# Kernel tuning notes

Hardware: AMD Instinct MI355X
Metric: run time of the kernel (lower is better)

Reference implementation:

```python
import jax, jax.numpy as jnp
import numpy as np
import math

M, INPUT_DIM, CLASSES, LATENT = 4096, 64, 10, 2

# ---- Bessel-approximation phi functions (Abramowitz & Stegun polynomial series) ----

def phi_f(s):
    t = s / 7.5
    t2 = t * t
    poly = 1.0 + 3.5156229 * t2 + 3.0899424 * t2**2 + 1.2067492 * t2**3 \
         + 0.2659732 * t2**4 + 0.0360768 * t2**5 + 0.0045813 * t2**6
    return jnp.exp(-s / 2.0) * poly


def phi_g(s):
    t = s / 7.5
    u = 1.0 / t  # s >= 7.5 when called via phi, so t >= 1
    poly = 0.39894228 + 0.01328592 * u + 0.00225319 * u**2 - 0.00157565 * u**3 \
         + 0.0091628 * u**4 - 0.02057706 * u**5 + 0.02635537 * u**6 \
         - 0.01647633 * u**7 + 0.00392377 * u**8
    return jnp.sqrt(2.0 / s) * poly


def phi(x):
    a = jnp.float32(7.5)
    return phi_f(jnp.minimum(x, a)) - phi_f(a) + phi_g(jnp.maximum(x, a))


def phi_d(s, D):
    if D <= 2:
        return phi(s)
    return 1.0 / jnp.sqrt(1.0 + 4.0 * s / (2 * D - 3))


def cramer_wold_distance(X, mu, variance, p, gamma):
    m, K = X.shape
    variance_matrix = variance[None, :] + variance[:, None]          # [C, C]
    # A term: pairwise latent-sample distances [m, m]
    A1 = jnp.sum((X[None, :, :] - X[:, None, :]) ** 2, axis=-1)      # [m, m]
    A = jnp.sum(phi_d(A1 / (4.0 * gamma), K)) / (m * m * math.sqrt(2.0 * math.pi * 2.0 * gamma))
    # B term: sample-to-mean distances [m, C]
    B1 = jnp.sum((mu[None, :, :] - X[:, None, :]) ** 2, axis=-1)     # [m, C]
    B2 = phi_d(B1 / (2.0 * (variance + 2.0 * gamma)), K)
    B = jnp.sum(2.0 * p / (m * jnp.sqrt(2.0 * math.pi * (variance + 2.0 * gamma))) * B2)
    # C term: mean-to-mean distances [C, C]
    C1 = jnp.sum((mu[None, :, :] - mu[:, None, :]) ** 2, axis=-1)
    C2 = phi_d(C1 / (2.0 * variance_matrix + 4.0 * gamma), K)
    C3 = jnp.outer(p, p) / jnp.sqrt(2.0 * math.pi * (variance_matrix + 2.0 * gamma))
    C = jnp.sum(C3 * C2)
    return A - B + C


def setup_inputs() -> dict:
    key = jax.random.key(0)
    ks = jax.random.split(key, 12)
    tau = jax.random.normal(ks[0], (M, INPUT_DIM), dtype=jnp.float32)
    # first half of batch is labeled (one-hot), second half unlabeled (zeros)
    lab_idx = jax.random.randint(ks[1], (M // 2,), 0, CLASSES)
    labels = jnp.concatenate([jax.nn.one_hot(lab_idx, CLASSES, dtype=jnp.float32),
                              jnp.zeros((M - M // 2, CLASSES), jnp.float32)], axis=0)
    batch_data = jnp.concatenate([tau, labels], axis=1)

    def xavier(k, fan_in, fan_out):
        lim = math.sqrt(6.0 / (fan_in + fan_out))
        return jax.random.uniform(k, (fan_in, fan_out), jnp.float32, -lim, lim)

    inp = {
        'batch_data': batch_data,
        'We1': xavier(ks[2], INPUT_DIM, 32), 'be1': jnp.zeros((32,), jnp.float32),
        'We2': xavier(ks[3], 32, 16),        'be2': jnp.zeros((16,), jnp.float32),
        'We3': xavier(ks[4], 16, LATENT),    'be3': jnp.zeros((LATENT,), jnp.float32),
        'Wd1': xavier(ks[5], LATENT, 16),    'bd1': jnp.zeros((16,), jnp.float32),
        'Wd2': xavier(ks[6], 16, 32),        'bd2': jnp.zeros((32,), jnp.float32),
        'Wd3': xavier(ks[7], 32, INPUT_DIM), 'bd3': jnp.zeros((INPUT_DIM,), jnp.float32),
        # GMM: init=2.0, gauss_num <= z_dim branch not taken (10 > 2) -> N(0, init)
        'means': 2.0 * jax.random.normal(ks[8], (CLASSES, LATENT), jnp.float32),
        'variances': jnp.ones((CLASSES,), jnp.float32),
        'probs': jnp.full((CLASSES,), 1.0 / CLASSES, jnp.float32),
    }
    return inp


def segma_forward(batch_data, We1, be1, We2, be2, We3, be3,
                  Wd1, bd1, Wd2, bd2, Wd3, bd3, means, variances, probs):
    tau = batch_data[:, :INPUT_DIM]
    labels = batch_data[:, INPUT_DIM:]
    # encoder
    x = jnp.tanh(tau @ We1 + be1)
    x = jnp.tanh(x @ We2 + be2)
    z = x @ We3 + be3                                               # [m, K]
    # decoder
    h = jnp.tanh(z @ Wd1 + bd1)
    h = jnp.tanh(h @ Wd2 + bd2)
    tau_decoded = h @ Wd3 + bd3
    rec_loss = jnp.mean((tau - tau_decoded) ** 2)
    # labeled mask: rows whose one-hot labels sum to exactly 1
    labeled_mask = (jnp.sum(labels, axis=-1) == 1.0)
    # class logits: Gaussian log-likelihood under each mixture component
    D = means.shape[-1]
    sq = jnp.sum((z[:, None, :] - means[None, :, :]) ** 2, axis=-1)  # [m, C]
    class_logits = jnp.log(probs) - 0.5 * D * jnp.log(2.0 * math.pi * variances) - sq / (2.0 * variances)
    # cross-entropy with (soft/one-hot) float targets, masked to labeled rows
    ce = -jnp.sum(labels * jax.nn.log_softmax(class_logits, axis=-1), axis=-1)
    den = jnp.sum(labels)
    den = jnp.where(den == 0, 1.0, den)
    class_loss = jnp.sum(ce * labeled_mask.astype(jnp.float32)) / den
    # Cramer-Wold cost (train_labeled=True -> use all z)
    m = z.shape[0]
    gamma = jnp.float32((4.0 / (3.0 * m)) ** 0.2)
    cw_cost = cramer_wold_distance(z, means, variances, probs, gamma)
    log_cw_cost = 8.0 + jnp.log(cw_cost)
    total_loss = rec_loss + 1.0 * log_cw_cost + 2.0 * class_loss
    return total_loss


def reference(batch_data, We1, be1, We2, be2, We3, be3,
              Wd1, bd1, Wd2, bd2, Wd3, bd3, means, variances, probs):
    return segma_forward(batch_data, We1, be1, We2, be2, We3, be3,
                         Wd1, bd1, Wd2, bd2, Wd3, bd3, means, variances, probs)
```

## Files before the change

### kernel.cpp

```cpp
#include <hip/hip_runtime.h>
#include <math.h>

#define M_ROWS 4096
#define IN_DIM 64
#define NCLS 10
#define ROW_STRIDE 74
#define TWO_PI_F 6.283185307179586f
#define NTILE 64
#define NPAIR 2080
#define NBLK_MLP 256

__device__ __forceinline__ float phi_f_eval(float s) {
    float t = s * (1.0f / 7.5f);
    float t2 = t * t;
    float p = 0.0045813f;
    p = fmaf(p, t2, 0.0360768f);
    p = fmaf(p, t2, 0.2659732f);
    p = fmaf(p, t2, 1.2067492f);
    p = fmaf(p, t2, 3.0899424f);
    p = fmaf(p, t2, 3.5156229f);
    p = fmaf(p, t2, 1.0f);
    return __expf(-0.5f * s) * p;
}

__device__ __forceinline__ float phi_g_eval(float s) {
    float r = __builtin_amdgcn_rcpf(s);
    float u = 7.5f * r;
    float p = 0.00392377f;
    p = fmaf(p, u, -0.01647633f);
    p = fmaf(p, u, 0.02635537f);
    p = fmaf(p, u, -0.02057706f);
    p = fmaf(p, u, 0.0091628f);
    p = fmaf(p, u, -0.00157565f);
    p = fmaf(p, u, 0.00225319f);
    p = fmaf(p, u, 0.01328592f);
    p = fmaf(p, u, 0.39894228f);
    return __builtin_amdgcn_sqrtf(2.0f * r) * p;
}

#define PHI_F_75 0.21445709f

__device__ __forceinline__ float phi_eval(float s) {
    float f = phi_f_eval(fminf(s, 7.5f));
    float g = phi_g_eval(fmaxf(s, 7.5f));
    return f - PHI_F_75 + g;
}

__device__ __forceinline__ float fast_tanh(float x) {
    float e = __expf(2.0f * x);
    float r = __builtin_amdgcn_rcpf(e + 1.0f);
    return fmaf(-2.0f, r, 1.0f);
}

__device__ __forceinline__ float waveReduce(float v) {
    v += __shfl_down(v, 32, 64);
    v += __shfl_down(v, 16, 64);
    v += __shfl_down(v, 8, 64);
    v += __shfl_down(v, 4, 64);
    v += __shfl_down(v, 2, 64);
    v += __shfl_down(v, 1, 64);
    return v;
}

__device__ __forceinline__ double waveReduceD(double v) {
    v += __shfl_down(v, 32, 64);
    v += __shfl_down(v, 16, 64);
    v += __shfl_down(v, 8, 64);
    v += __shfl_down(v, 4, 64);
    v += __shfl_down(v, 2, 64);
    v += __shfl_down(v, 1, 64);
    return v;
}

__device__ __forceinline__ float sel4(float v0, float v1, float v2, float v3, int r) {
    float a = (r & 1) ? v1 : v0;
    float b = (r & 1) ? v3 : v2;
    return (r & 2) ? b : a;
}

#define P_W1   0
#define P_W2   2304
#define P_WD2  2944
#define P_WD3  3520
#define P_W3   5696
#define P_WD1  5728
#define P_B1   5760
#define P_B2   5792
#define P_B3   5808
#define P_BD1  5810
#define P_BD2  5826
#define P_BD3  5858
#define P_MU   5922
#define P_VAR  5942
#define P_PRB  5952
#define SMT    5962

__global__ __launch_bounds__(64, 1) void k_mlp(
    const float* __restrict__ batch,
    const float* __restrict__ We1, const float* __restrict__ be1,
    const float* __restrict__ We2, const float* __restrict__ be2,
    const float* __restrict__ We3, const float* __restrict__ be3,
    const float* __restrict__ Wd1, const float* __restrict__ bd1,
    const float* __restrict__ Wd2, const float* __restrict__ bd2,
    const float* __restrict__ Wd3, const float* __restrict__ bd3,
    const float* __restrict__ means, const float* __restrict__ vars,
    const float* __restrict__ probs,
    float2* __restrict__ zbuf,
    float* __restrict__ recp, float* __restrict__ Bp,
    float* __restrict__ clsp, float* __restrict__ labp,
    float gamma)
{
    __shared__ __align__(16) float sm[SMT];
    const int tid = threadIdx.x;

    for (int idx = tid; idx < 2048; idx += 64) { int i = idx >> 5, j = idx & 31; sm[P_W1  + i * 36 + j] = We1[idx]; }
    for (int idx = tid; idx < 512;  idx += 64) { int i = idx >> 4, j = idx & 15; sm[P_W2  + i * 20 + j] = We2[idx]; }
    for (int idx = tid; idx < 512;  idx += 64) { int i = idx >> 5, j = idx & 31; sm[P_WD2 + i * 36 + j] = Wd2[idx]; }
    for (int idx = tid; idx < 2048; idx += 64) { int i = idx >> 6, j = idx & 63; sm[P_WD3 + i * 68 + j] = Wd3[idx]; }
    if (tid < 32) sm[P_W3 + tid] = We3[tid];
    else          sm[P_WD1 + tid - 32] = Wd1[tid - 32];
    if (tid < 32) sm[P_B1 + tid] = be1[tid];
    if (tid < 16) sm[P_B2 + tid] = be2[tid];
    if (tid < 2)  sm[P_B3 + tid] = be3[tid];
    if (tid < 16) sm[P_BD1 + tid] = bd1[tid];
    if (tid < 32) sm[P_BD2 + tid] = bd2[tid];
    sm[P_BD3 + tid] = bd3[tid];
    if (tid < 20) sm[P_MU + tid] = means[tid];
    if (tid < 10) sm[P_VAR + tid] = vars[tid];
    if (tid < 10) sm[P_PRB + tid] = probs[tid];
    __syncthreads();

    const int rw = tid & 15;
    const int r  = tid >> 4;
    const int row = blockIdx.x * 16 + rw;
    const float* rp = batch + (size_t)row * ROW_STRIDE;

    float taus[16];
#pragma unroll
    for (int k = 0; k < 16; k++) taus[k] = rp[r + 4 * k];

    float a1[32];
#pragma unroll
    for (int j = 0; j < 32; j++) a1[j] = 0.0f;
#pragma unroll
    for (int k = 0; k < 16; k++) {
        const int i = r + 4 * k;
        const float4* wr = (const float4*)&sm[P_W1 + i * 36];
        const float ti = taus[k];
#pragma unroll
        for (int jj = 0; jj < 8; jj++) {
            float4 w = wr[jj];
            a1[4 * jj + 0] = fmaf(ti, w.x, a1[4 * jj + 0]);
            a1[4 * jj + 1] = fmaf(ti, w.y, a1[4 * jj + 1]);
            a1[4 * jj + 2] = fmaf(ti, w.z, a1[4 * jj + 2]);
            a1[4 * jj + 3] = fmaf(ti, w.w, a1[4 * jj + 3]);
        }
    }
#pragma unroll
    for (int j = 0; j < 32; j++) {
        a1[j] += __shfl_xor(a1[j], 16, 64);
        a1[j] += __shfl_xor(a1[j], 32, 64);
    }
    float x1own[8];
#pragma unroll
    for (int k = 0; k < 8; k++)
        x1own[k] = fast_tanh(sel4(a1[4 * k], a1[4 * k + 1], a1[4 * k + 2], a1[4 * k + 3], r)
                             + sm[P_B1 + r + 4 * k]);

    float a2[16];
#pragma unroll
    for (int j = 0; j < 16; j++) a2[j] = 0.0f;
#pragma unroll
    for (int k = 0; k < 8; k++) {
        const int i = r + 4 * k;
        const float4* wr = (const float4*)&sm[P_W2 + i * 20];
        const float x = x1own[k];
#pragma unroll
        for (int jj = 0; jj < 4; jj++) {
            float4 w = wr[jj];
            a2[4 * jj + 0] = fmaf(x, w.x, a2[4 * jj + 0]);
            a2[4 * jj + 1] = fmaf(x, w.y, a2[4 * jj + 1]);
            a2[4 * jj + 2] = fmaf(x, w.z, a2[4 * jj + 2]);
            a2[4 * jj + 3] = fmaf(x, w.w, a2[4 * jj + 3]);
        }
    }
#pragma unroll
    for (int j = 0; j < 16; j++) {
        a2[j] += __shfl_xor(a2[j], 16, 64);
        a2[j] += __shfl_xor(a2[j], 32, 64);
    }
    float x2own[4];
#pragma unroll
    for (int k = 0; k < 4; k++)
        x2own[k] = fast_tanh(sel4(a2[4 * k], a2[4 * k + 1], a2[4 * k + 2], a2[4 * k + 3], r)
                             + sm[P_B2 + r + 4 * k]);

    float z0 = 0.0f, z1 = 0.0f;
#pragma unroll
    for (int k = 0; k < 4; k++) {
        const int i = r + 4 * k;
        z0 = fmaf(x2own[k], sm[P_W3 + 2 * i], z0);
        z1 = fmaf(x2own[k], sm[P_W3 + 2 * i + 1], z1);
    }
    z0 += __shfl_xor(z0, 16, 64); z0 += __shfl_xor(z0, 32, 64);
    z1 += __shfl_xor(z1, 16, 64); z1 += __shfl_xor(z1, 32, 64);
    z0 += sm[P_B3 + 0];
    z1 += sm[P_B3 + 1];
    if (r == 0) zbuf[row] = make_float2(z0, z1);

    float h1own[4];
#pragma unroll
    for (int k = 0; k < 4; k++) {
        const int j = r + 4 * k;
        float acc = sm[P_BD1 + j];
        acc = fmaf(z0, sm[P_WD1 + j], acc);
        acc = fmaf(z1, sm[P_WD1 + 16 + j], acc);
        h1own[k] = fast_tanh(acc);
    }

    float a3[32];
#pragma unroll
    for (int j = 0; j < 32; j++) a3[j] = 0.0f;
#pragma unroll
    for (int k = 0; k < 4; k++) {
        const int i = r + 4 * k;
        const float4* wr = (const float4*)&sm[P_WD2 + i * 36];
        const float x = h1own[k];
#pragma unroll
        for (int jj = 0; jj < 8; jj++) {
            float4 w = wr[jj];
            a3[4 * jj + 0] = fmaf(x, w.x, a3[4 * jj + 0]);
            a3[4 * jj + 1] = fmaf(x, w.y, a3[4 * jj + 1]);
            a3[4 * jj + 2] = fmaf(x, w.z, a3[4 * jj + 2]);
            a3[4 * jj + 3] = fmaf(x, w.w, a3[4 * jj + 3]);
        }
    }
#pragma unroll
    for (int j = 0; j < 32; j++) {
        a3[j] += __shfl_xor(a3[j], 16, 64);
        a3[j] += __shfl_xor(a3[j], 32, 64);
    }
    float h2own[8];
#pragma unroll
    for (int k = 0; k < 8; k++)
        h2own[k] = fast_tanh(sel4(a3[4 * k], a3[4 * k + 1], a3[4 * k + 2], a3[4 * k + 3], r)
                             + sm[P_BD2 + r + 4 * k]);

    float a4[64];
#pragma unroll
    for (int j = 0; j < 64; j++) a4[j] = 0.0f;
#pragma unroll
    for (int k = 0; k < 8; k++) {
        const int i = r + 4 * k;
        const float4* wr = (const float4*)&sm[P_WD3 + i * 68];
        const float x = h2own[k];
#pragma unroll
        for (int jj = 0; jj < 16; jj++) {
            float4 w = wr[jj];
            a4[4 * jj + 0] = fmaf(x, w.x, a4[4 * jj + 0]);
            a4[4 * jj + 1] = fmaf(x, w.y, a4[4 * jj + 1]);
            a4[4 * jj + 2] = fmaf(x, w.z, a4[4 * jj + 2]);
            a4[4 * jj + 3] = fmaf(x, w.w, a4[4 * jj + 3]);
        }
    }
#pragma unroll
    for (int j = 0; j < 64; j++) {
        a4[j] += __shfl_xor(a4[j], 16, 64);
        a4[j] += __shfl_xor(a4[j], 32, 64);
    }
    float rec = 0.0f;
#pragma unroll
    for (int k = 0; k < 16; k++) {
        float dec = sel4(a4[4 * k], a4[4 * k + 1], a4[4 * k + 2], a4[4 * k + 3], r)
                    + sm[P_BD3 + r + 4 * k];
        float e = dec - taus[k];
        rec = fmaf(e, e, rec);
    }

    const float two_g = 2.0f * gamma;
    const float inv_m = 1.0f / (float)M_ROWS;
    float lg[NCLS];
    float mx = -3.0e38f;
    float Bacc = 0.0f;
#pragma unroll
    for (int c = 0; c < NCLS; c++) {
        float d0 = z0 - sm[P_MU + 2 * c];
        float d1 = z1 - sm[P_MU + 2 * c + 1];
        float sqc = fmaf(d0, d0, d1 * d1);
        float vc = sm[P_VAR + c];
        float lgc = __logf(sm[P_PRB + c]) - __logf(TWO_PI_F * vc)
                    - sqc * 0.5f * __builtin_amdgcn_rcpf(vc);
        lg[c] = lgc;
        mx = fmaxf(mx, lgc);

        float den = vc + two_g;
        float sB = sqc * 0.5f * __builtin_amdgcn_rcpf(den);
        float coef = 2.0f * inv_m * sm[P_PRB + c] * __builtin_amdgcn_rsqf(TWO_PI_F * den);
        Bacc = fmaf(coef, phi_eval(sB), Bacc);
    }
    float esum = 0.0f;
#pragma unroll
    for (int c = 0; c < NCLS; c++) esum += __expf(lg[c] - mx);
    float lse = __logf(esum) + mx;

    float suml = 0.0f, ce = 0.0f;
#pragma unroll
    for (int c = 0; c < NCLS; c++) {
        float lb = rp[IN_DIM + c];
        suml += lb;
        ce = fmaf(lb, lse - lg[c], ce);
    }
    float cls = (suml == 1.0f) ? ce : 0.0f;
    if (r != 0) { Bacc = 0.0f; cls = 0.0f; suml = 0.0f; }

    float r0 = waveReduce(rec);
    float r1 = waveReduce(Bacc);
    float r2 = waveReduce(cls);
    float r3 = waveReduce(suml);
    if (tid == 0) {
        recp[blockIdx.x] = r0;
        Bp[blockIdx.x]   = r1;
        clsp[blockIdx.x] = r2;
        labp[blockIdx.x] = r3;
    }
}

__global__ __launch_bounds__(64, 4) void k_pair(
    const float2* __restrict__ z, float* __restrict__ Apart, float inv4g)
{
    const int p = blockIdx.x;
    int tj = (int)((__builtin_amdgcn_sqrtf(8.0f * (float)p + 1.0f) - 1.0f) * 0.5f);
    while ((tj + 1) * (tj + 2) / 2 <= p) tj++;
    while (tj * (tj + 1) / 2 > p) tj--;
    const int ti = p - tj * (tj + 1) / 2;

    const int lane = threadIdx.x;
    __shared__ float2 zjs[64];
    float2 zi = z[ti * 64 + lane];
    zjs[lane] = z[tj * 64 + lane];
    __syncthreads();

    float acc0 = 0.0f, acc1 = 0.0f;
#pragma unroll 8
    for (int jj = 0; jj < 64; jj += 2) {
        float2 a = zjs[jj], b = zjs[jj + 1];
        float dx0 = zi.x - a.x, dy0 = zi.y - a.y;
        float dx1 = zi.x - b.x, dy1 = zi.y - b.y;
        acc0 += phi_eval(fmaf(dx0, dx0, dy0 * dy0) * inv4g);
        acc1 += phi_eval(fmaf(dx1, dx1, dy1 * dy1) * inv4g);
    }
    float tot = waveReduce(acc0 + acc1);
    if (lane == 0) Apart[p] = (ti == tj) ? tot : 2.0f * tot;
}

__global__ __launch_bounds__(256) void k_fin(
    const float* __restrict__ means, const float* __restrict__ vars,
    const float* __restrict__ probs,
    const float* __restrict__ Apart,
    const float* __restrict__ recp, const float* __restrict__ Bp,
    const float* __restrict__ clsp, const float* __restrict__ labp,
    float* __restrict__ out, float gamma)
{
    __shared__ double wsum[8];
    const int t = threadIdx.x;
    const int w = t >> 6;
    const int l = t & 63;

    const double m = (double)M_ROWS;
    const double gam = (double)gamma;
    const double invA = 1.0 / (m * m * sqrt(2.0 * M_PI * 2.0 * gam));

    double av = 0.0;
#pragma unroll
    for (int k = 0; k < 9; k++) {
        int idx = t + 256 * k;
        if (idx < NPAIR) av += (double)Apart[idx];
    }

    double cv = 0.0;
    if (t < 100) {
        int ci = t / 10, cj = t - 10 * (t / 10);
        float vm = vars[ci] + vars[cj];
        float d0 = means[2 * ci] - means[2 * cj];
        float d1 = means[2 * ci + 1] - means[2 * cj + 1];
        float c1 = fmaf(d0, d0, d1 * d1);
        float s = c1 / (2.0f * vm + 4.0f * gamma);
        float c2 = phi_eval(s);
        float c3 = probs[ci] * probs[cj] * __builtin_amdgcn_rsqf(TWO_PI_F * (vm + 2.0f * gamma));
        cv = (double)(c3 * c2);
    }

    double acw = waveReduceD(av * invA + cv);

    const float* arr = (w == 0) ? recp : (w == 1) ? Bp : (w == 2) ? clsp : labp;
    double pv = 0.0;
#pragma unroll
    for (int k = 0; k < 4; k++) pv += (double)arr[l + 64 * k];
    double pw = waveReduceD(pv);

    if (l == 0) { wsum[w] = acw; wsum[4 + w] = pw; }
    __syncthreads();

    if (t == 0) {
        double AC = wsum[0] + wsum[1] + wsum[2] + wsum[3];
        double rec = wsum[4], B = wsum[5], cls = wsum[6], lab = wsum[7];
        double den = (lab == 0.0) ? 1.0 : lab;
        double cw = AC - B;
        double total = rec / (m * 64.0) + 8.0 + log(cw) + 2.0 * (cls / den);
        out[0] = (float)total;
    }
}

extern "C" void kernel_launch(void* const* d_in, const int* in_sizes, int n_in,
                              void* d_out, int out_size, void* d_ws, size_t ws_size,
                              hipStream_t stream) {
    (void)in_sizes; (void)n_in; (void)out_size; (void)ws_size;
    const float* batch = (const float*)d_in[0];
    const float* We1 = (const float*)d_in[1];
    const float* be1 = (const float*)d_in[2];
    const float* We2 = (const float*)d_in[3];
    const float* be2 = (const float*)d_in[4];
    const float* We3 = (const float*)d_in[5];
    const float* be3 = (const float*)d_in[6];
    const float* Wd1 = (const float*)d_in[7];
    const float* bd1 = (const float*)d_in[8];
    const float* Wd2 = (const float*)d_in[9];
    const float* bd2 = (const float*)d_in[10];
    const float* Wd3 = (const float*)d_in[11];
    const float* bd3 = (const float*)d_in[12];
    const float* means = (const float*)d_in[13];
    const float* vars = (const float*)d_in[14];
    const float* probs = (const float*)d_in[15];

    float* ws = (float*)d_ws;
    float2* zbuf = (float2*)ws;
    float* Apart = ws + 8192;
    float* recp  = ws + 12288;
    float* Bp    = ws + 12544;
    float* clsp  = ws + 12800;
    float* labp  = ws + 13056;

    const float gamma = (float)pow(4.0 / (3.0 * (double)M_ROWS), 0.2);
    const float inv4g = 1.0f / (4.0f * gamma);

    k_mlp<<<NBLK_MLP, 64, 0, stream>>>(batch, We1, be1, We2, be2, We3, be3,
                                       Wd1, bd1, Wd2, bd2, Wd3, bd3,
                                       means, vars, probs,
                                       zbuf, recp, Bp, clsp, labp, gamma);
    k_pair<<<NPAIR, 64, 0, stream>>>(zbuf, Apart, inv4g);
    k_fin<<<1, 256, 0, stream>>>(means, vars, probs, Apart, recp, Bp, clsp, labp,
                                 (float*)d_out, gamma);
}
```

Before: 116.9 us.

## Split MLP rows across 8 lane groups and fold final reduction into pair kernel

The MLP kernel now handles 8 rows per block across 512 blocks instead of 16 rows across 256, so each lane group reduces over 8 partial sums with an extra shuffle stage. The per-row class and B-term math now runs only on the owner lanes. The separate finalize kernel is removed: the last pair block, detected with an atomic counter reset by the MLP kernel, does the global reduction, saving one kernel launch. This adds atomics and fences, more shuffle traffic per block, and a single-wave tail reduction over all partials.

New measurement: 155.3 us. 1.33x slower.

```diff
diff --git a/kernel.cpp b/kernel.cpp
--- a/kernel.cpp
+++ b/kernel.cpp
@@ -6,9 +6,8 @@
 #define NCLS 10
 #define ROW_STRIDE 74
 #define TWO_PI_F 6.283185307179586f
-#define NTILE 64
 #define NPAIR 2080
-#define NBLK_MLP 256
+#define NBLK_MLP 512
 
 __device__ __forceinline__ float phi_f_eval(float s) {
     float t = s * (1.0f / 7.5f);
@@ -76,6 +75,12 @@
     float a = (r & 1) ? v1 : v0;
     float b = (r & 1) ? v3 : v2;
     return (r & 2) ? b : a;
+}
+__device__ __forceinline__ float sel8(float v0, float v1, float v2, float v3,
+                                      float v4, float v5, float v6, float v7, int r) {
+    float a = sel4(v0, v1, v2, v3, r);
+    float b = sel4(v4, v5, v6, v7, r);
+    return (r & 4) ? b : a;
 }
 
 #define P_W1   0
@@ -108,10 +113,13 @@
     float2* __restrict__ zbuf,
     float* __restrict__ recp, float* __restrict__ Bp,
     float* __restrict__ clsp, float* __restrict__ labp,
+    int* __restrict__ cnt,
     float gamma)
 {
     __shared__ __align__(16) float sm[SMT];
     const int tid = threadIdx.x;
+
+    if (blockIdx.x == 0 && tid == 0) *cnt = 0;
 
     for (int idx = tid; idx < 2048; idx += 64) { int i = idx >> 5, j = idx & 31; sm[P_W1  + i * 36 + j] = We1[idx]; }
     for (int idx = tid; idx < 512;  idx += 64) { int i = idx >> 4, j = idx & 15; sm[P_W2  + i * 20 + j] = We2[idx]; }
@@ -130,21 +138,21 @@
     if (tid < 10) sm[P_PRB + tid] = probs[tid];
     __syncthreads();
 
-    const int rw = tid & 15;
-    const int r  = tid >> 4;
-    const int row = blockIdx.x * 16 + rw;
+    const int rw = tid & 7;
+    const int r  = tid >> 3;
+    const int row = blockIdx.x * 8 + rw;
     const float* rp = batch + (size_t)row * ROW_STRIDE;
 
-    float taus[16];
-#pragma unroll
-    for (int k = 0; k < 16; k++) taus[k] = rp[r + 4 * k];
+    float taus[8];
+#pragma unroll
+    for (int k = 0; k < 8; k++) taus[k] = rp[r + 8 * k];
 
     float a1[32];
 #pragma unroll
     for (int j = 0; j < 32; j++) a1[j] = 0.0f;
 #pragma unroll
-    for (int k = 0; k < 16; k++) {
-        const int i = r + 4 * k;
+    for (int k = 0; k < 8; k++) {
+        const int i = r + 8 * k;
         const float4* wr = (const float4*)&sm[P_W1 + i * 36];
         const float ti = taus[k];
 #pragma unroll
@@ -158,21 +166,23 @@
     }
 #pragma unroll
     for (int j = 0; j < 32; j++) {
+        a1[j] += __shfl_xor(a1[j], 8, 64);
         a1[j] += __shfl_xor(a1[j], 16, 64);
         a1[j] += __shfl_xor(a1[j], 32, 64);
     }
-    float x1own[8];
-#pragma unroll
-    for (int k = 0; k < 8; k++)
-        x1own[k] = fast_tanh(sel4(a1[4 * k], a1[4 * k + 1], a1[4 * k + 2], a1[4 * k + 3], r)
-                             + sm[P_B1 + r + 4 * k]);
+    float x1own[4];
+#pragma unroll
+    for (int k = 0; k < 4; k++)
+        x1own[k] = fast_tanh(sel8(a1[8 * k], a1[8 * k + 1], a1[8 * k + 2], a1[8 * k + 3],
+                                  a1[8 * k + 4], a1[8 * k + 5], a1[8 * k + 6], a1[8 * k + 7], r)
+                             + sm[P_B1 + r + 8 * k]);
 
     float a2[16];
 #pragma unroll
     for (int j = 0; j < 16; j++) a2[j] = 0.0f;
 #pragma unroll
-    for (int k = 0; k < 8; k++) {
-        const int i = r + 4 * k;
+    for (int k = 0; k < 4; k++) {
+        const int i = r + 8 * k;
         const float4* wr = (const float4*)&sm[P_W2 + i * 20];
         const float x = x1own[k];
 #pragma unroll
@@ -186,32 +196,34 @@
     }
 #pragma unroll
     for (int j = 0; j < 16; j++) {
+        a2[j] += __shfl_xor(a2[j], 8, 64);
         a2[j] += __shfl_xor(a2[j], 16, 64);
         a2[j] += __shfl_xor(a2[j], 32, 64);
     }
-    float x2own[4];
-#pragma unroll
-    for (int k = 0; k < 4; k++)
-        x2own[k] = fast_tanh(sel4(a2[4 * k], a2[4 * k + 1], a2[4 * k + 2], a2[4 * k + 3], r)
-                             + sm[P_B2 + r + 4 * k]);
+    float x2own[2];
+#pragma unroll
+    for (int k = 0; k < 2; k++)
+        x2own[k] = fast_tanh(sel8(a2[8 * k], a2[8 * k + 1], a2[8 * k + 2], a2[8 * k + 3],
+                                  a2[8 * k + 4], a2[8 * k + 5], a2[8 * k + 6], a2[8 * k + 7], r)
+                             + sm[P_B2 + r + 8 * k]);
 
     float z0 = 0.0f, z1 = 0.0f;
 #pragma unroll
-    for (int k = 0; k < 4; k++) {
-        const int i = r + 4 * k;
+    for (int k = 0; k < 2; k++) {
+        const int i = r + 8 * k;
         z0 = fmaf(x2own[k], sm[P_W3 + 2 * i], z0);
         z1 = fmaf(x2own[k], sm[P_W3 + 2 * i + 1], z1);
     }
-    z0 += __shfl_xor(z0, 16, 64); z0 += __shfl_xor(z0, 32, 64);
-    z1 += __shfl_xor(z1, 16, 64); z1 += __shfl_xor(z1, 32, 64);
+    z0 += __shfl_xor(z0, 8, 64); z0 += __shfl_xor(z0, 16, 64); z0 += __shfl_xor(z0, 32, 64);
+    z1 += __shfl_xor(z1, 8, 64); z1 += __shfl_xor(z1, 16, 64); z1 += __shfl_xor(z1, 32, 64);
     z0 += sm[P_B3 + 0];
     z1 += sm[P_B3 + 1];
     if (r == 0) zbuf[row] = make_float2(z0, z1);
 
-    float h1own[4];
-#pragma unroll
-    for (int k = 0; k < 4; k++) {
-        const int j = r + 4 * k;
+    float h1own[2];
+#pragma unroll
+    for (int k = 0; k < 2; k++) {
+        const int j = r + 8 * k;
         float acc = sm[P_BD1 + j];
         acc = fmaf(z0, sm[P_WD1 + j], acc);
         acc = fmaf(z1, sm[P_WD1 + 16 + j], acc);
@@ -222,8 +234,8 @@
 #pragma unroll
     for (int j = 0; j < 32; j++) a3[j] = 0.0f;
 #pragma unroll
-    for (int k = 0; k < 4; k++) {
-        const int i = r + 4 * k;
+    for (int k = 0; k < 2; k++) {
+        const int i = r + 8 * k;
         const float4* wr = (const float4*)&sm[P_WD2 + i * 36];
         const float x = h1own[k];
 #pragma unroll
@@ -237,21 +249,23 @@
     }
 #pragma unroll
     for (int j = 0; j < 32; j++) {
+        a3[j] += __shfl_xor(a3[j], 8, 64);
         a3[j] += __shfl_xor(a3[j], 16, 64);
         a3[j] += __shfl_xor(a3[j], 32, 64);
     }
-    float h2own[8];
-#pragma unroll
-    for (int k = 0; k < 8; k++)
-        h2own[k] = fast_tanh(sel4(a3[4 * k], a3[4 * k + 1], a3[4 * k + 2], a3[4 * k + 3], r)
-                             + sm[P_BD2 + r + 4 * k]);
+    float h2own[4];
+#pragma unroll
+    for (int k = 0; k < 4; k++)
+        h2own[k] = fast_tanh(sel8(a3[8 * k], a3[8 * k + 1], a3[8 * k + 2], a3[8 * k + 3],
+                                  a3[8 * k + 4], a3[8 * k + 5], a3[8 * k + 6], a3[8 * k + 7], r)
+                             + sm[P_BD2 + r + 8 * k]);
 
     float a4[64];
 #pragma unroll
     for (int j = 0; j < 64; j++) a4[j] = 0.0f;
 #pragma unroll
-    for (int k = 0; k < 8; k++) {
-        const int i = r + 4 * k;
+    for (int k = 0; k < 4; k++) {
+        const int i = r + 8 * k;
         const float4* wr = (const float4*)&sm[P_WD3 + i * 68];
         const float x = h2own[k];
 #pragma unroll
@@ -265,53 +279,56 @@
     }
 #pragma unroll
     for (int j = 0; j < 64; j++) {
+        a4[j] += __shfl_xor(a4[j], 8, 64);
         a4[j] += __shfl_xor(a4[j], 16, 64);
         a4[j] += __shfl_xor(a4[j], 32, 64);
     }
     float rec = 0.0f;
 #pragma unroll
-    for (int k = 0; k < 16; k++) {
-        float dec = sel4(a4[4 * k], a4[4 * k + 1], a4[4 * k + 2], a4[4 * k + 3], r)
-                    + sm[P_BD3 + r + 4 * k];
+    for (int k = 0; k < 8; k++) {
+        float dec = sel8(a4[8 * k], a4[8 * k + 1], a4[8 * k + 2], a4[8 * k + 3],
+                         a4[8 * k + 4], a4[8 * k + 5], a4[8 * k + 6], a4[8 * k + 7], r)
+                    + sm[P_BD3 + r + 8 * k];
         float e = dec - taus[k];
         rec = fmaf(e, e, rec);
     }
 
-    const float two_g = 2.0f * gamma;
-    const float inv_m = 1.0f / (float)M_ROWS;
-    float lg[NCLS];
-    float mx = -3.0e38f;
-    float Bacc = 0.0f;
-#pragma unroll
-    for (int c = 0; c < NCLS; c++) {
-        float d0 = z0 - sm[P_MU + 2 * c];
-        float d1 = z1 - sm[P_MU + 2 * c + 1];
-        float sqc = fmaf(d0, d0, d1 * d1);
-        float vc = sm[P_VAR + c];
-        float lgc = __logf(sm[P_PRB + c]) - __logf(TWO_PI_F * vc)
-                    - sqc * 0.5f * __builtin_amdgcn_rcpf(vc);
-        lg[c] = lgc;
-        mx = fmaxf(mx, lgc);
-
-        float den = vc + two_g;
-        float sB = sqc * 0.5f * __builtin_amdgcn_rcpf(den);
-        float coef = 2.0f * inv_m * sm[P_PRB + c] * __builtin_amdgcn_rsqf(TWO_PI_F * den);
-        Bacc = fmaf(coef, phi_eval(sB), Bacc);
-    }
-    float esum = 0.0f;
-#pragma unroll
-    for (int c = 0; c < NCLS; c++) esum += __expf(lg[c] - mx);
-    float lse = __logf(esum) + mx;
-
-    float suml = 0.0f, ce = 0.0f;
-#pragma unroll
-    for (int c = 0; c < NCLS; c++) {
-        float lb = rp[IN_DIM + c];
-        suml += lb;
-        ce = fmaf(lb, lse - lg[c], ce);
-    }
-    float cls = (suml == 1.0f) ? ce : 0.0f;
-    if (r != 0) { Bacc = 0.0f; cls = 0.0f; suml = 0.0f; }
+    float Bacc = 0.0f, cls = 0.0f, suml = 0.0f;
+    if (r == 0) {
+        const float two_g = 2.0f * gamma;
+        const float inv_m = 1.0f / (float)M_ROWS;
+        float lg[NCLS];
+        float mx = -3.0e38f;
+#pragma unroll
+        for (int c = 0; c < NCLS; c++) {
+            float d0 = z0 - sm[P_MU + 2 * c];
+            float d1 = z1 - sm[P_MU + 2 * c + 1];
+            float sqc = fmaf(d0, d0, d1 * d1);
+            float vc = sm[P_VAR + c];
+            float lgc = __logf(sm[P_PRB + c]) - __logf(TWO_PI_F * vc)
+                        - sqc * 0.5f * __builtin_amdgcn_rcpf(vc);
+            lg[c] = lgc;
+            mx = fmaxf(mx, lgc);
+
+            float den = vc + two_g;
+            float sB = sqc * 0.5f * __builtin_amdgcn_rcpf(den);
+            float coef = 2.0f * inv_m * sm[P_PRB + c] * __builtin_amdgcn_rsqf(TWO_PI_F * den);
+            Bacc = fmaf(coef, phi_eval(sB), Bacc);
+        }
+        float esum = 0.0f;
+#pragma unroll
+        for (int c = 0; c < NCLS; c++) esum += __expf(lg[c] - mx);
+        float lse = __logf(esum) + mx;
+
+        float ce = 0.0f;
+#pragma unroll
+        for (int c = 0; c < NCLS; c++) {
+            float lb = rp[IN_DIM + c];
+            suml += lb;
+            ce = fmaf(lb, lse - lg[c], ce);
+        }
+        cls = (suml == 1.0f) ? ce : 0.0f;
+    }
 
     float r0 = waveReduce(rec);
     float r1 = waveReduce(Bacc);
@@ -326,7 +343,13 @@
 }
 
 __global__ __launch_bounds__(64, 4) void k_pair(
-    const float2* __restrict__ z, float* __restrict__ Apart, float inv4g)
+    const float2* __restrict__ z, float* __restrict__ Apart,
+    const float* __restrict__ recp, const float* __restrict__ Bp,
+    const float* __restrict__ clsp, const float* __restrict__ labp,
+    const float* __restrict__ means, const float* __restrict__ vars,
+    const float* __restrict__ probs,
+    float* __restrict__ out, int* __restrict__ cnt,
+    float inv4g, float gamma)
 {
     const int p = blockIdx.x;
     int tj = (int)((__builtin_amdgcn_sqrtf(8.0f * (float)p + 1.0f) - 1.0f) * 0.5f);
@@ -350,21 +373,17 @@
         acc1 += phi_eval(fmaf(dx1, dx1, dy1 * dy1) * inv4g);
     }
     float tot = waveReduce(acc0 + acc1);
-    if (lane == 0) Apart[p] = (ti == tj) ? tot : 2.0f * tot;
-}
-
-__global__ __launch_bounds__(256) void k_fin(
-    const float* __restrict__ means, const float* __restrict__ vars,
-    const float* __restrict__ probs,
-    const float* __restrict__ Apart,
-    const float* __restrict__ recp, const float* __restrict__ Bp,
-    const float* __restrict__ clsp, const float* __restrict__ labp,
-    float* __restrict__ out, float gamma)
-{
-    __shared__ double wsum[8];
-    const int t = threadIdx.x;
-    const int w = t >> 6;
-    const int l = t & 63;
+
+    int old = 0;
+    if (lane == 0) {
+        Apart[p] = (ti == tj) ? tot : 2.0f * tot;
+        __threadfence();
+        old = atomicAdd(cnt, 1);
+    }
+    old = __shfl(old, 0, 64);
+    if (old != NPAIR - 1) return;
+
+    __threadfence();
 
     const double m = (double)M_ROWS;
     const double gam = (double)gamma;
@@ -372,13 +391,13 @@
 
     double av = 0.0;
 #pragma unroll
-    for (int k = 0; k < 9; k++) {
-        int idx = t + 256 * k;
+    for (int k = 0; k < 33; k++) {
+        int idx = lane + 64 * k;
         if (idx < NPAIR) av += (double)Apart[idx];
     }
 
     double cv = 0.0;
-    if (t < 100) {
+    for (int t = lane; t < 100; t += 64) {
         int ci = t / 10, cj = t - 10 * (t / 10);
         float vm = vars[ci] + vars[cj];
         float d0 = means[2 * ci] - means[2 * cj];
@@ -387,23 +406,26 @@
         float s = c1 / (2.0f * vm + 4.0f * gamma);
         float c2 = phi_eval(s);
         float c3 = probs[ci] * probs[cj] * __builtin_amdgcn_rsqf(TWO_PI_F * (vm + 2.0f * gamma));
-        cv = (double)(c3 * c2);
-    }
-
-    double acw = waveReduceD(av * invA + cv);
-
-    const float* arr = (w == 0) ? recp : (w == 1) ? Bp : (w == 2) ? clsp : labp;
-    double pv = 0.0;
-#pragma unroll
-    for (int k = 0; k < 4; k++) pv += (double)arr[l + 64 * k];
-    double pw = waveReduceD(pv);
-
-    if (l == 0) { wsum[w] = acw; wsum[4 + w] = pw; }
-    __syncthreads();
-
-    if (t == 0) {
-        double AC = wsum[0] + wsum[1] + wsum[2] + wsum[3];
-        double rec = wsum[4], B = wsum[5], cls = wsum[6], lab = wsum[7];
+        cv += (double)(c3 * c2);
+    }
+
+    double rec = 0.0, B = 0.0, cls = 0.0, lab = 0.0;
+#pragma unroll
+    for (int k = 0; k < 8; k++) {
+        int idx = lane + 64 * k;
+        rec += (double)recp[idx];
+        B   += (double)Bp[idx];
+        cls += (double)clsp[idx];
+        lab += (double)labp[idx];
+    }
+
+    double AC = waveReduceD(av * invA + cv);
+    rec = waveReduceD(rec);
+    B   = waveReduceD(B);
+    cls = waveReduceD(cls);
+    lab = waveReduceD(lab);
+
+    if (lane == 0) {
         double den = (lab == 0.0) ? 1.0 : lab;
         double cw = AC - B;
         double total = rec / (m * 64.0) + 8.0 + log(cw) + 2.0 * (cls / den);
@@ -436,9 +458,10 @@
     float2* zbuf = (float2*)ws;
     float* Apart = ws + 8192;
     float* recp  = ws + 12288;
-    float* Bp    = ws + 12544;
-    float* clsp  = ws + 12800;
-    float* labp  = ws + 13056;
+    float* Bp    = ws + 12800;
+    float* clsp  = ws + 13312;
+    float* labp  = ws + 13824;
+    int*   cnt   = (int*)(ws + 14336);
 
     const float gamma = (float)pow(4.0 / (3.0 * (double)M_ROWS), 0.2);
     const float inv4g = 1.0f / (4.0f * gamma);
@@ -446,8 +469,8 @@
     k_mlp<<<NBLK_MLP, 64, 0, stream>>>(batch, We1, be1, We2, be2, We3, be3,
                                        Wd1, bd1, Wd2, bd2, Wd3, bd3,
                                        means, vars, probs,
-                                       zbuf, recp, Bp, clsp, labp, gamma);
-    k_pair<<<NPAIR, 64, 0, stream>>>(zbuf, Apart, inv4g);
-    k_fin<<<1, 256, 0, stream>>>(means, vars, probs, Apart, recp, Bp, clsp, labp,
-                                 (float*)d_out, gamma);
-}
+                                       zbuf, recp, Bp, clsp, labp, cnt, gamma);
+    k_pair<<<NPAIR, 64, 0, stream>>>(zbuf, Apart, recp, Bp, clsp, labp,
+                                     means, vars, probs,
+                                     (float*)d_out, cnt, inv4g, gamma);
+}
```
